# Kernel optimization log

Measured on AMD Instinct MI355X. Metric: run time of the kernel, lower is better.

The kernel has to match this reference:

```python
import jax, jax.numpy as jnp
import numpy as np

B, L, S, H, E = 2, 2048, 2048, 8, 64

def setup_inputs() -> dict:
    key = jax.random.key(0)
    k1, k2, k3 = jax.random.split(key, 3)
    queries = jax.random.normal(k1, (B, L, H, E), dtype=jnp.float32)
    keys = jax.random.normal(k2, (B, S, H, E), dtype=jnp.float32)
    values = jax.random.normal(k3, (B, S, H, E), dtype=jnp.float32)
    # TriangularCausalMask: True above the diagonal (positions to mask out)
    attn_mask = jnp.broadcast_to(
        jnp.triu(jnp.ones((L, S), dtype=bool), k=1)[None, None], (B, 1, L, S)
    )
    return {"queries": queries, "keys": keys, "values": values, "attn_mask": attn_mask}

def reference(queries, keys, values, attn_mask):
    E_ = queries.shape[-1]
    scale = 1.0 / (E_ ** 0.5)  # self.scale is None -> 1/sqrt(E)
    # scores: [B, H, L, S]
    scores = jnp.einsum('blhe,bshe->bhls', queries, keys)
    scores = jnp.where(attn_mask, -jnp.inf, scores)  # masked_fill_(mask, -inf)
    series = jax.nn.softmax(scale * scores, axis=-1)  # dropout p=0.0 -> identity
    V = jnp.einsum('bhls,bshd->blhd', series, values)
    return V, series
```

## Files before the change

kernel.cpp:

```cpp
#include <hip/hip_runtime.h>
#include <hip/hip_bf16.h>

typedef __attribute__((ext_vector_type(8))) short bf16x8;
typedef __attribute__((ext_vector_type(4))) short s16x4;
typedef __attribute__((ext_vector_type(4))) float f32x4;

constexpr int B = 2, L = 2048, S = 2048, H = 8, E = 64;
constexpr int TL = 64;
constexpr int SN = 64;
constexpr int LDK = 72;
constexpr int THREADS = 256;
constexpr int GSTR = H * E;

__device__ __forceinline__ float bf2f(short s) {
  union { unsigned u; float f; } c; c.u = ((unsigned)(unsigned short)s) << 16;
  return c.f;
}
__device__ __forceinline__ short f2bf(float x) {
  union { float f; unsigned u; } c; c.f = x;
  unsigned r = c.u + 0x7fffu + ((c.u >> 16) & 1u);
  return (short)(r >> 16);
}
__device__ __forceinline__ f32x4 mk4(float a, float b, float c, float d) {
  f32x4 v; v[0] = a; v[1] = b; v[2] = c; v[3] = d; return v;
}

struct Tile16 { f32x4 v0, v1, v2, v3; };

__device__ __forceinline__ void ld_tile(const float* __restrict__ g, int tid, Tile16& t) {
  const int r = tid >> 2, c = (tid & 3) * 16;
  const f32x4* q = (const f32x4*)(g + (size_t)r * GSTR + c);
  t.v0 = q[0]; t.v1 = q[1]; t.v2 = q[2]; t.v3 = q[3];
}

__device__ __forceinline__ void cvt_tile(const Tile16& t, short* __restrict__ o) {
  float vv[16] = { t.v0[0],t.v0[1],t.v0[2],t.v0[3], t.v1[0],t.v1[1],t.v1[2],t.v1[3],
                   t.v2[0],t.v2[1],t.v2[2],t.v2[3], t.v3[0],t.v3[1],t.v3[2],t.v3[3] };
#pragma unroll
  for (int k = 0; k < 8; ++k) {
    __hip_bfloat162 h = __float22bfloat162_rn(make_float2(vv[2*k], vv[2*k+1]));
    short2 s2 = *(short2*)&h;
    o[2*k] = s2.x; o[2*k+1] = s2.y;
  }
}

__device__ __forceinline__ void stK(const Tile16& t, short (* __restrict__ Kb)[LDK], int tid) {
  const int r = tid >> 2, c = (tid & 3) * 16;
  short s[16]; cvt_tile(t, s);
  *(bf16x8*)&Kb[r][c]     = *(bf16x8*)&s[0];
  *(bf16x8*)&Kb[r][c + 8] = *(bf16x8*)&s[8];
}

__device__ __forceinline__ void stV(const Tile16& t, short (* __restrict__ Vb)[LDK], int tid) {
  const int sr = tid >> 2, c = (tid & 3) * 16;
  short s[16]; cvt_tile(t, s);
#pragma unroll
  for (int i = 0; i < 16; ++i) {
    const int e = c + i;
    Vb[e][sr ^ (8 * ((e >> 3) & 7))] = s[i];
  }
}

__device__ __forceinline__ bf16x8 cvt8(f32x4 u0, f32x4 u1) {
  short o[8];
  float vv[8] = { u0[0],u0[1],u0[2],u0[3], u1[0],u1[1],u1[2],u1[3] };
#pragma unroll
  for (int k = 0; k < 4; ++k) {
    __hip_bfloat162 h = __float22bfloat162_rn(make_float2(vv[2*k], vv[2*k+1]));
    short2 s2 = *(short2*)&h;
    o[2*k] = s2.x; o[2*k+1] = s2.y;
  }
  return *(bf16x8*)o;
}

__device__ __forceinline__ int swz_t(int raw) {
  return (raw & 1) ? (31 - (raw >> 1)) : (raw >> 1);
}

__global__ __launch_bounds__(THREADS, 2)
void k_rowsum(const float* __restrict__ Q, const float* __restrict__ K,
              float* __restrict__ outV, float* __restrict__ outS,
              float* __restrict__ ws)
{
  __shared__ __align__(16) short Qs[TL][LDK];
  __shared__ __align__(16) short Ks[2][SN][LDK];

  const int tid  = threadIdx.x;
  const int lane = tid & 63;
  const int wv   = tid >> 6;
  const int quad = lane >> 4;
  const int n16  = lane & 15;

  const int t  = swz_t(blockIdx.x >> 1);
  const int hh = blockIdx.x & 1;
  const int bh = blockIdx.y;
  const int b = bh >> 3, h = bh & 7;
  const int l0 = t * TL;
  const int s_hi = l0 + TL;
  const int nt = s_hi / SN;
  const int st0 = hh ? (nt + 1) / 2 : 0;
  const int st1 = hh ? nt : (nt + 1) / 2;

  const size_t qbase = ((size_t)b * L * H + h) * E;
  const size_t kbase = ((size_t)b * S * H + h) * E;
  const size_t srow  = (size_t)bh * L * S;

  {
    const f32x4 z = {0.f, 0.f, 0.f, 0.f};
#pragma unroll
    for (int i = 0; i < 2; ++i) {
      const int idx = tid * 2 + i;
      const int r = (idx >> 4) + hh * 32, c = idx & 15;
      *(f32x4*)(outV + qbase + (size_t)(l0 + r) * GSTR + c * 4) = z;
    }
  }

  {
    const int s4lo = s_hi / 4;
    const int mid  = s4lo + (((S / 4 - s4lo) >> 1) & ~15);
    const int lo = hh ? mid : s4lo;
    const int hi = hh ? S / 4 : mid;
    const f32x4 z = {0.f, 0.f, 0.f, 0.f};
    for (int r = 0; r < TL; ++r) {
      f32x4* p = (f32x4*)(outS + srow + (size_t)(l0 + r) * S);
      for (int s4 = lo + tid; s4 < hi; s4 += THREADS)
        __builtin_nontemporal_store(z, p + s4);
    }
  }

  Tile16 pk;
  if (st0 < st1)
    ld_tile(K + kbase + (size_t)st0 * SN * GSTR, tid, pk);
  {
    Tile16 tq;
    ld_tile(Q + qbase + (size_t)l0 * GSTR, tid, tq);
    stK(tq, Qs, tid);
  }
  __syncthreads();

  bf16x8 a0 = *(const bf16x8*)&Qs[wv * 16 + n16][quad * 8];
  bf16x8 a1 = *(const bf16x8*)&Qs[wv * 16 + n16][32 + quad * 8];

  float rsum[4] = {0.f, 0.f, 0.f, 0.f};
  for (int st = st0; st < st1; ++st) {
    short (*Kb)[LDK] = Ks[(st - st0) & 1];
    stK(pk, Kb, tid);
    if (st + 1 < st1)
      ld_tile(K + kbase + (size_t)(st + 1) * SN * GSTR, tid, pk);
    __syncthreads();

    const int s0 = st * SN;
#pragma unroll
    for (int nn = 0; nn < 4; ++nn) {
      bf16x8 b0 = *(const bf16x8*)&Kb[nn * 16 + n16][quad * 8];
      bf16x8 b1 = *(const bf16x8*)&Kb[nn * 16 + n16][32 + quad * 8];
      f32x4 acc = {0.f, 0.f, 0.f, 0.f};
      acc = __builtin_amdgcn_mfma_f32_16x16x32_bf16(a0, b0, acc, 0, 0, 0);
      acc = __builtin_amdgcn_mfma_f32_16x16x32_bf16(a1, b1, acc, 0, 0, 0);
#pragma unroll
      for (int r = 0; r < 4; ++r) {
        const int l = l0 + wv * 16 + quad * 4 + r;
        const int s = s0 + nn * 16 + n16;
        rsum[r] += (s <= l) ? __expf(acc[r] * 0.125f) : 0.f;
      }
    }
    __syncthreads();
  }

#pragma unroll
  for (int r = 0; r < 4; ++r)
#pragma unroll
    for (int off = 1; off < 16; off <<= 1)
      rsum[r] += __shfl_xor(rsum[r], off, 64);
  if (n16 == 0)
#pragma unroll
    for (int r = 0; r < 4; ++r)
      ws[(size_t)(hh * B * H + bh) * L + l0 + wv * 16 + quad * 4 + r] = rsum[r];
}

__global__ __launch_bounds__(THREADS, 3)
void k_pv(const float* __restrict__ Q, const float* __restrict__ K,
          const float* __restrict__ V, float* __restrict__ outV,
          float* __restrict__ outS, const float* __restrict__ ws)
{
  __shared__ __align__(16) short Ks[2][SN][LDK];
  __shared__ __align__(16) short Vt[2][E][LDK];
  __shared__ __align__(16) short Ps[4][16][LDK];

  const int tid  = threadIdx.x;
  const int lane = tid & 63;
  const int wv   = tid >> 6;
  const int quad = lane >> 4;
  const int n16  = lane & 15;

  const int t    = swz_t(blockIdx.x >> 2);
  const int part = blockIdx.x & 3;
  const int bh = blockIdx.y;
  const int b = bh >> 3, h = bh & 7;
  const int l0 = t * TL;
  const int nt = (l0 + TL) / SN;
  const int st0 = (part * nt) >> 2;
  const int st1 = ((part + 1) * nt) >> 2;
  if (st0 >= st1) return;

  const size_t qbase = ((size_t)b * L * H + h) * E;
  const size_t kbase = ((size_t)b * S * H + h) * E;
  const size_t srow  = (size_t)bh * L * S;

  const int qrow = l0 + wv * 16 + n16;
  const float* qp = Q + qbase + (size_t)qrow * GSTR;
  bf16x8 a0 = cvt8(*(const f32x4*)(qp + quad * 8), *(const f32x4*)(qp + quad * 8 + 4));
  bf16x8 a1 = cvt8(*(const f32x4*)(qp + 32 + quad * 8), *(const f32x4*)(qp + 36 + quad * 8));

  float inv_r[4];
#pragma unroll
  for (int r = 0; r < 4; ++r) {
    const size_t idx = (size_t)l0 + wv * 16 + quad * 4 + r;
    inv_r[r] = 1.f / (ws[(size_t)bh * L + idx] + ws[(size_t)(B * H + bh) * L + idx]);
  }

  f32x4 oacc[4] = {{0,0,0,0},{0,0,0,0},{0,0,0,0},{0,0,0,0}};

  Tile16 pk2, pv2;
  ld_tile(K + kbase + (size_t)st0 * SN * GSTR, tid, pk2);
  ld_tile(V + kbase + (size_t)st0 * SN * GSTR, tid, pv2);

  for (int st = st0; st < st1; ++st) {
    const int s0 = st * SN;
    const int buf = (st - st0) & 1;
    short (*Kb)[LDK] = Ks[buf];
    short (*Vb)[LDK] = Vt[buf];
    stK(pk2, Kb, tid);
    stV(pv2, Vb, tid);
    if (st + 1 < st1) {
      ld_tile(K + kbase + (size_t)(st + 1) * SN * GSTR, tid, pk2);
      ld_tile(V + kbase + (size_t)(st + 1) * SN * GSTR, tid, pv2);
    }
    __syncthreads();

#pragma unroll
    for (int nn = 0; nn < 4; ++nn) {
      bf16x8 b0 = *(const bf16x8*)&Kb[nn * 16 + n16][quad * 8];
      bf16x8 b1 = *(const bf16x8*)&Kb[nn * 16 + n16][32 + quad * 8];
      f32x4 acc = {0.f, 0.f, 0.f, 0.f};
      acc = __builtin_amdgcn_mfma_f32_16x16x32_bf16(a0, b0, acc, 0, 0, 0);
      acc = __builtin_amdgcn_mfma_f32_16x16x32_bf16(a1, b1, acc, 0, 0, 0);
#pragma unroll
      for (int r = 0; r < 4; ++r) {
        const int l = l0 + wv * 16 + quad * 4 + r;
        const int s = s0 + nn * 16 + n16;
        float w = (s <= l) ? __expf(acc[r] * 0.125f) * inv_r[r] : 0.f;
        Ps[wv][quad * 4 + r][(nn * 16 + n16) ^ (8 * quad)] = f2bf(w);
      }
    }

    asm volatile("s_waitcnt lgkmcnt(0)" ::: "memory");

    {
      const int row = lane >> 2;
      const int sub = lane & 3;
      const int swz = 8 * (lane >> 4);
      float* dstrow = outS + srow + (size_t)(l0 + wv * 16 + row) * S + s0;
#pragma unroll
      for (int i = 0; i < 4; ++i) {
        const int c = (i * 16 + sub * 4) ^ swz;
        s16x4 pw = *(const s16x4*)&Ps[wv][row][c];
        f32x4 o = mk4(bf2f(pw[0]), bf2f(pw[1]), bf2f(pw[2]), bf2f(pw[3]));
        __builtin_nontemporal_store(o, (f32x4*)(dstrow + i * 16 + sub * 4));
      }
    }

    {
      const int psw = 8 * ((n16 >> 2) & 3);
      bf16x8 pa0 = *(const bf16x8*)&Ps[wv][n16][(quad * 8)      ^ psw];
      bf16x8 pa1 = *(const bf16x8*)&Ps[wv][n16][(32 + quad * 8) ^ psw];
#pragma unroll
      for (int nn = 0; nn < 4; ++nn) {
        const int e   = nn * 16 + n16;
        const int vsw = 8 * ((e >> 3) & 7);
        bf16x8 vb0 = *(const bf16x8*)&Vb[e][(quad * 8)      ^ vsw];
        bf16x8 vb1 = *(const bf16x8*)&Vb[e][(32 + quad * 8) ^ vsw];
        oacc[nn] = __builtin_amdgcn_mfma_f32_16x16x32_bf16(pa0, vb0, oacc[nn], 0, 0, 0);
        oacc[nn] = __builtin_amdgcn_mfma_f32_16x16x32_bf16(pa1, vb1, oacc[nn], 0, 0, 0);
      }
    }
    __syncthreads();
  }

#pragma unroll
  for (int nn = 0; nn < 4; ++nn)
#pragma unroll
    for (int r = 0; r < 4; ++r) {
      const int l = l0 + wv * 16 + quad * 4 + r;
      atomicAdd(&outV[qbase + (size_t)l * GSTR + nn * 16 + n16], oacc[nn][r]);
    }
}

extern "C" void kernel_launch(void* const* d_in, const int* in_sizes, int n_in,
                              void* d_out, int out_size, void* d_ws, size_t ws_size,
                              hipStream_t stream) {
  const float* Q = (const float*)d_in[0];
  const float* K = (const float*)d_in[1];
  const float* V = (const float*)d_in[2];
  float* outV = (float*)d_out;
  float* outS = outV + (size_t)B * L * H * E;
  float* inv  = (float*)d_ws;
  k_rowsum<<<dim3(2 * L / TL, B * H), THREADS, 0, stream>>>(Q, K, outV, outS, inv);
  k_pv<<<dim3(4 * L / TL, B * H), THREADS, 0, stream>>>(Q, K, V, outV, outS, inv);
}
```

Before: 390.4 us.

## Load Q directly into registers and store softmax probabilities straight from MFMA output

The rowsum kernel now loads Q fragments straight from global memory into registers and converts them there, dropping the Qs shared tile and a barrier, and its launch bound rises to 3 blocks per SM. The output kernel writes the fp32 softmax weights to the series output directly from the MFMA accumulators with scalar nontemporal stores, instead of reading bf16 back from LDS and writing float4. The stored probabilities are now unrounded fp32 rather than bf16-rounded. The trade is coalesced 16-byte stores replaced by strided 4-byte stores, plus possible register pressure from the higher occupancy target.

```diff
diff --git a/kernel.cpp b/kernel.cpp
--- a/kernel.cpp
+++ b/kernel.cpp
@@ -2,7 +2,6 @@
 #include <hip/hip_bf16.h>
 
 typedef __attribute__((ext_vector_type(8))) short bf16x8;
-typedef __attribute__((ext_vector_type(4))) short s16x4;
 typedef __attribute__((ext_vector_type(4))) float f32x4;
 
 constexpr int B = 2, L = 2048, S = 2048, H = 8, E = 64;
@@ -12,17 +11,10 @@
 constexpr int THREADS = 256;
 constexpr int GSTR = H * E;
 
-__device__ __forceinline__ float bf2f(short s) {
-  union { unsigned u; float f; } c; c.u = ((unsigned)(unsigned short)s) << 16;
-  return c.f;
-}
 __device__ __forceinline__ short f2bf(float x) {
   union { float f; unsigned u; } c; c.f = x;
   unsigned r = c.u + 0x7fffu + ((c.u >> 16) & 1u);
   return (short)(r >> 16);
-}
-__device__ __forceinline__ f32x4 mk4(float a, float b, float c, float d) {
-  f32x4 v; v[0] = a; v[1] = b; v[2] = c; v[3] = d; return v;
 }
 
 struct Tile16 { f32x4 v0, v1, v2, v3; };
@@ -77,12 +69,11 @@
   return (raw & 1) ? (31 - (raw >> 1)) : (raw >> 1);
 }
 
-__global__ __launch_bounds__(THREADS, 2)
+__global__ __launch_bounds__(THREADS, 3)
 void k_rowsum(const float* __restrict__ Q, const float* __restrict__ K,
               float* __restrict__ outV, float* __restrict__ outS,
               float* __restrict__ ws)
 {
-  __shared__ __align__(16) short Qs[TL][LDK];
   __shared__ __align__(16) short Ks[2][SN][LDK];
 
   const int tid  = threadIdx.x;
@@ -131,15 +122,10 @@
   Tile16 pk;
   if (st0 < st1)
     ld_tile(K + kbase + (size_t)st0 * SN * GSTR, tid, pk);
-  {
-    Tile16 tq;
-    ld_tile(Q + qbase + (size_t)l0 * GSTR, tid, tq);
-    stK(tq, Qs, tid);
-  }
-  __syncthreads();
-
-  bf16x8 a0 = *(const bf16x8*)&Qs[wv * 16 + n16][quad * 8];
-  bf16x8 a1 = *(const bf16x8*)&Qs[wv * 16 + n16][32 + quad * 8];
+  const int qrow = l0 + wv * 16 + n16;
+  const float* qp = Q + qbase + (size_t)qrow * GSTR;
+  bf16x8 a0 = cvt8(*(const f32x4*)(qp + quad * 8), *(const f32x4*)(qp + quad * 8 + 4));
+  bf16x8 a1 = cvt8(*(const f32x4*)(qp + 32 + quad * 8), *(const f32x4*)(qp + 36 + quad * 8));
 
   float rsum[4] = {0.f, 0.f, 0.f, 0.f};
   for (int st = st0; st < st1; ++st) {
@@ -238,6 +224,7 @@
     }
     __syncthreads();
 
+    float* srow0 = outS + srow + (size_t)(l0 + wv * 16) * S + s0;
 #pragma unroll
     for (int nn = 0; nn < 4; ++nn) {
       bf16x8 b0 = *(const bf16x8*)&Kb[nn * 16 + n16][quad * 8];
@@ -250,25 +237,13 @@
         const int l = l0 + wv * 16 + quad * 4 + r;
         const int s = s0 + nn * 16 + n16;
         float w = (s <= l) ? __expf(acc[r] * 0.125f) * inv_r[r] : 0.f;
+        __builtin_nontemporal_store(w,
+            srow0 + (size_t)(quad * 4 + r) * S + nn * 16 + n16);
         Ps[wv][quad * 4 + r][(nn * 16 + n16) ^ (8 * quad)] = f2bf(w);
       }
     }
 
     asm volatile("s_waitcnt lgkmcnt(0)" ::: "memory");
-
-    {
-      const int row = lane >> 2;
-      const int sub = lane & 3;
-      const int swz = 8 * (lane >> 4);
-      float* dstrow = outS + srow + (size_t)(l0 + wv * 16 + row) * S + s0;
-#pragma unroll
-      for (int i = 0; i < 4; ++i) {
-        const int c = (i * 16 + sub * 4) ^ swz;
-        s16x4 pw = *(const s16x4*)&Ps[wv][row][c];
-        f32x4 o = mk4(bf2f(pw[0]), bf2f(pw[1]), bf2f(pw[2]), bf2f(pw[3]));
-        __builtin_nontemporal_store(o, (f32x4*)(dstrow + i * 16 + sub * 4));
-      }
-    }
 
     {
       const int psw = 8 * ((n16 >> 2) & 3);
```

Result: no change. 391.5 us (+0.3%).
